# Kernel tuning notes

Measured on AMD Instinct MI355X. Metric: run time of the kernel, lower is better.

## Reference

```python
import jax, jax.numpy as jnp
import numpy as np

THRESH = 0.4


def setup_inputs() -> dict:
    key = jax.random.key(0)
    ks = jax.random.split(key, 8)
    B, N, C, H, O = 8, 16384, 640, 256, 128
    s = 0.02  # small init so sigmoid(logits) ~ 0.5 -> realistic mixed selection
    return {
        "point_features": jax.random.normal(ks[0], (B, N, C), jnp.float32),
        "point_coords": jax.random.normal(ks[1], (B, N, 3), jnp.float32) * 10.0,
        "w1": jax.random.normal(ks[2], (C, H), jnp.float32) * s,
        "b1": jnp.zeros((H,), jnp.float32),
        "w2": jax.random.normal(ks[3], (H, 1), jnp.float32) * s,
        "b2": jnp.zeros((1,), jnp.float32),
        "wo": jax.random.normal(ks[4], (C, O), jnp.float32) * s,
        "bo": jnp.zeros((O,), jnp.float32),
    }


def reference(point_features, point_coords, w1, b1, w2, b2, wo, bo):
    B, N, _ = point_features.shape
    # 2-layer MLP -> per-point logit -> sigmoid score
    h = jax.nn.relu(jnp.einsum('bnc,ch->bnh', point_features, w1) + b1)
    logits = jnp.einsum('bnh,ho->bno', h, w2) + b2          # [B, N, 1]
    scores = jax.nn.sigmoid(logits)                          # [B, N, 1]
    # score-scaled features through output projection
    feats = jnp.einsum('bnc,co->bno', point_features * scores, wo) + bo  # [B, N, O]
    # score-threshold selection + per-batch stream compaction into a
    # zero-padded tensor (padded to N, the jit-static worst case)
    sel = scores[..., 0] > THRESH                            # [B, N] bool
    pos = jnp.cumsum(sel.astype(jnp.int32), axis=1) - 1      # destination slot
    pos = jnp.where(sel, pos, N)                             # unselected -> OOB (dropped)
    bidx = jnp.arange(B)[:, None]
    selected_keypoints = jnp.zeros_like(feats).at[bidx, pos].set(feats, mode='drop')
    selected_coords = jnp.zeros_like(point_coords).at[bidx, pos].set(point_coords, mode='drop')
    # point_mask: True where the row is zero padding (matches (coords==0).sum(-1)!=0)
    point_mask = jnp.sum(selected_coords == 0, axis=-1) != 0
    return selected_keypoints, selected_coords, point_mask
```

## Files before the change

kernel.cpp:

```cpp
#include <hip/hip_runtime.h>
#include <hip/hip_bf16.h>


typedef __attribute__((ext_vector_type(8))) short short8v;
typedef __attribute__((ext_vector_type(4))) float f32x4;

#define M_TOTAL 131072
#define C_DIM 640
#define H_DIM 256
#define O_DIM 128
#define NCOMB 384
#define TM 64
#define KSTEPS 20
#define N_PTS 16384
#define TILES_PER_B 256
#define NTILES 2048
#define THRL -0.4054651081f
#define FIX_MARGIN 0.03f

#define OUT_COORD_OFF 16777216
#define OUT_MASK_OFF  17170432

#define WT_OFF     0u
#define TSTATE_OFF 491520u
#define TICKET_OFF 507904u
#define COUNTS_OFF 507908u

__device__ __forceinline__ int swzA(int u) {
  return u ^ (((u >> 3) & 1) | (((u >> 6) & 3) << 1));
}
__device__ __forceinline__ int swzB(int u) { return u ^ ((u >> 3) & 7); }

__device__ __forceinline__ void glds16(const void* g, void* l) {
  const __attribute__((address_space(1))) unsigned int* gp =
      reinterpret_cast<const __attribute__((address_space(1))) unsigned int*>(
          reinterpret_cast<uintptr_t>(g));
  __attribute__((address_space(3))) unsigned int* lp =
      reinterpret_cast<__attribute__((address_space(3))) unsigned int*>(
          reinterpret_cast<uintptr_t>(l));
  __builtin_amdgcn_global_load_lds(gp, lp, 16, 0, 0);
}

__device__ __forceinline__ unsigned int f2bf_bits(float f) {
  unsigned int u = __builtin_bit_cast(unsigned int, f);
  return (u + 0x7fffu + ((u >> 16) & 1u)) >> 16;
}
__device__ __forceinline__ unsigned int pack_bf2(float lo, float hi) {
  return f2bf_bits(lo) | (f2bf_bits(hi) << 16);
}

__global__ __launch_bounds__(256) void convert_w(const float* __restrict__ w1,
                                                 const float* __restrict__ wo,
                                                 unsigned short* __restrict__ Wt2,
                                                 unsigned long long* __restrict__ tstate,
                                                 int* __restrict__ ticket) {
  int o = blockIdx.x * 256 + threadIdx.x;
  if (o < NTILES) tstate[o] = 0ull;
  if (o == NTILES) *ticket = 0;
  if (o < NCOMB * C_DIM) {
    int e = o & 7;
    int chunk = o >> 3;
    int ks = chunk / 1536;
    int r = chunk - ks * 1536;
    int u = swzB(r);
    int n = u >> 2, kg = u & 3;
    int k = ks * 32 + kg * 8 + e;
    float v = (n < H_DIM) ? w1[k * H_DIM + n] : wo[k * O_DIM + (n - H_DIM)];
    Wt2[o] = (unsigned short)f2bf_bits(v);
  }
}

__global__ __launch_bounds__(512, 4) void gemm_fused(
    const float* __restrict__ pf, const unsigned short* __restrict__ Wt2,
    const float* __restrict__ w1, const float* __restrict__ b1,
    const float* __restrict__ w2, const float* __restrict__ b2,
    const float* __restrict__ pc, const float* __restrict__ bo,
    unsigned long long* __restrict__ tstate, int* __restrict__ ticket,
    int* __restrict__ counts, float* __restrict__ out) {
  __shared__ __align__(16) unsigned short As[2][256 * 8];
  __shared__ __align__(16) unsigned short Bs[2][1536 * 8];
  __shared__ float lpart[8][64];
  __shared__ float llog[64];
  __shared__ int dstrow[64];
  __shared__ float srow[64];
  __shared__ int s_tile;
  __shared__ unsigned long long s_fixmask;

  const int tid = threadIdx.x;
  const int lane = tid & 63;
  const int wv = tid >> 6;
  const int q = lane & 15;
  const int p = lane >> 4;

  if (tid == 0) s_tile = atomicAdd(ticket, 1);
  __syncthreads();
  const int tile = s_tile;
  const int m0 = tile * TM;

  f32x4 acc[3][4];
#pragma unroll
  for (int i = 0; i < 3; ++i)
#pragma unroll
    for (int rt = 0; rt < 4; ++rt) acc[i][rt] = (f32x4){0.f, 0.f, 0.f, 0.f};

  const int ar = tid >> 3;
  const int ah = tid & 7;
  const float* asrc = pf + (size_t)(m0 + ar) * C_DIM + ah * 4;
  const int awp = swzA(((ah >> 1) << 6) + ar) * 8 + (ah & 1) * 4;

  {
    float4 ra = *(const float4*)(asrc);
#pragma unroll
    for (int u = 0; u < 3; ++u)
      glds16(Wt2 + (size_t)(u * 512 + tid) * 8, &Bs[0][(u * 512 + tid) * 8]);
    *(uint2*)&As[0][awp] = make_uint2(pack_bf2(ra.x, ra.y), pack_bf2(ra.z, ra.w));
    __syncthreads();
  }

#pragma unroll 2
  for (int t = 0; t < KSTEPS; ++t) {
    const int cur = t & 1;
    float4 rn;
    if (t < KSTEPS - 1) {
      rn = *(const float4*)(asrc + (t + 1) * 32);
#pragma unroll
      for (int u = 0; u < 3; ++u)
        glds16(Wt2 + (size_t)((t + 1) * 1536 + u * 512 + tid) * 8,
               &Bs[cur ^ 1][(u * 512 + tid) * 8]);
    }
    short8v af[4];
#pragma unroll
    for (int rt = 0; rt < 4; ++rt)
      af[rt] = *(const short8v*)&As[cur][swzA((p << 6) + rt * 16 + q) * 8];
#pragma unroll
    for (int i = 0; i < 3; ++i) {
      const int ub = (((wv + 8 * i) * 16 + q) << 2) + p;
      short8v bfv = *(const short8v*)&Bs[cur][swzB(ub) * 8];
#pragma unroll
      for (int rt = 0; rt < 4; ++rt)
        acc[i][rt] = __builtin_amdgcn_mfma_f32_16x16x32_bf16(af[rt], bfv, acc[i][rt], 0, 0, 0);
    }
    if (t < KSTEPS - 1)
      *(uint2*)&As[cur ^ 1][awp] = make_uint2(pack_bf2(rn.x, rn.y), pack_bf2(rn.z, rn.w));
    __syncthreads();
  }

  float w2v[2], b1v[2];
#pragma unroll
  for (int i = 0; i < 2; ++i) {
    int col = (wv + 8 * i) * 16 + q;
    w2v[i] = w2[col];
    b1v[i] = b1[col];
  }
#pragma unroll
  for (int rt = 0; rt < 4; ++rt) {
    float pr[4] = {0.f, 0.f, 0.f, 0.f};
#pragma unroll
    for (int i = 0; i < 2; ++i)
#pragma unroll
      for (int r = 0; r < 4; ++r)
        pr[r] += fmaxf(acc[i][rt][r] + b1v[i], 0.f) * w2v[i];
#pragma unroll
    for (int mk = 1; mk < 16; mk <<= 1)
#pragma unroll
      for (int r = 0; r < 4; ++r) pr[r] += __shfl_xor(pr[r], mk);
    if (q == 0)
#pragma unroll
      for (int r = 0; r < 4; ++r) lpart[wv][rt * 16 + p * 4 + r] = pr[r];
  }
  __syncthreads();

  bool nf = false;
  if (wv == 0) {
    float lg = b2[0];
#pragma unroll
    for (int w = 0; w < 8; ++w) lg += lpart[w][tid];
    llog[tid] = lg;
    nf = fabsf(lg - THRL) < FIX_MARGIN;
  }
  unsigned long long fm = __ballot(nf);
  if (tid == 0) s_fixmask = fm;
  __syncthreads();

  unsigned long long fixmask = s_fixmask;
  while (fixmask) {
    int row = __ffsll(fixmask) - 1;
    fixmask &= fixmask - 1;
    if (tid < 256) {
      const float* prow = pf + (size_t)(m0 + row) * C_DIM;
      float a0 = 0.f, a1 = 0.f;
      for (int c = 0; c < C_DIM; c += 2) {
        a0 = fmaf(prow[c], w1[(size_t)c * H_DIM + tid], a0);
        a1 = fmaf(prow[c + 1], w1[(size_t)(c + 1) * H_DIM + tid], a1);
      }
      float v = fmaxf(a0 + a1 + b1[tid], 0.f) * w2[tid];
#pragma unroll
      for (int mk = 1; mk < 64; mk <<= 1) v += __shfl_xor(v, mk);
      if (lane == 0) lpart[0][wv] = v;
    }
    __syncthreads();
    if (tid == 0)
      llog[row] = lpart[0][0] + lpart[0][1] + lpart[0][2] + lpart[0][3] + b2[0];
    __syncthreads();
  }

  float flog = 0.f;
  bool sel = false;
  if (wv == 0) {
    flog = llog[tid];
    sel = flog > THRL;
  }
  unsigned long long selmask = __ballot(sel);
  if (wv == 0) {
    const int tb = tile & (TILES_PER_B - 1);
    const int cbase = tile - tb;
    int agg = __popcll(selmask);
    if (tid == 0) {
      unsigned long long fl = (tb == 0) ? 2ull : 1ull;
      __hip_atomic_store(&tstate[tile], (fl << 32) | (unsigned int)agg,
                         __ATOMIC_RELAXED, __HIP_MEMORY_SCOPE_AGENT);
    }
    int excl = 0;
    if (tb > 0) {
      int offset = tb - 1;
      while (true) {
        int idx = offset - tid;
        unsigned long long s = 0;
        if (idx >= 0) {
          do {
            s = __hip_atomic_load(&tstate[cbase + idx], __ATOMIC_RELAXED,
                                  __HIP_MEMORY_SCOPE_AGENT);
          } while (!(s >> 32));
        }
        unsigned flag = (unsigned)(s >> 32);
        unsigned long long pm = __ballot(flag == 2u);
        int val = (int)(s & 0xffffffffull);
        int contrib;
        if (pm) {
          int k = __ffsll(pm) - 1;
          contrib = (tid <= k) ? val : 0;
        } else {
          contrib = (idx >= 0) ? val : 0;
        }
#pragma unroll
        for (int mk = 1; mk < 64; mk <<= 1) contrib += __shfl_xor(contrib, mk);
        excl += contrib;
        if (pm) break;
        offset -= 64;
      }
      if (tid == 0)
        __hip_atomic_store(&tstate[tile], (2ull << 32) | (unsigned int)(excl + agg),
                           __ATOMIC_RELAXED, __HIP_MEMORY_SCOPE_AGENT);
    }
    int below = __popcll(selmask & ((1ull << tid) - 1ull));
    int bb = (tile >> 8) * N_PTS;
    dstrow[tid] = sel ? (bb + excl + below) : -1;
    srow[tid] = 1.f / (1.f + expf(-flog));
    if (tid == 0 && tb == TILES_PER_B - 1) counts[tile >> 8] = excl + agg;
  }
  __syncthreads();

  if (wv == 0 && dstrow[tid] >= 0) {
    int dst = dstrow[tid];
    int m = m0 + tid;
    float c0 = pc[m * 3], c1 = pc[m * 3 + 1], c2 = pc[m * 3 + 2];
    float* oc = out + OUT_COORD_OFF;
    oc[dst * 3] = c0; oc[dst * 3 + 1] = c1; oc[dst * 3 + 2] = c2;
    out[OUT_MASK_OFF + dst] = (c0 == 0.f || c1 == 0.f || c2 == 0.f) ? 1.f : 0.f;
  }

  {
    const int gcol = wv * 16 + q;
    const float bov = bo[gcol];
#pragma unroll
    for (int rt = 0; rt < 4; ++rt)
#pragma unroll
      for (int r = 0; r < 4; ++r) {
        int row = rt * 16 + p * 4 + r;
        int dst = dstrow[row];
        if (dst >= 0)
          out[(size_t)dst * O_DIM + gcol] = fmaf(acc[2][rt][r], srow[row], bov);
      }
  }
}

__global__ __launch_bounds__(256) void fill_tail(const int* __restrict__ counts,
                                                 float* __restrict__ out) {
  int m = blockIdx.x * 4 + (threadIdx.x >> 6);
  int lane = threadIdx.x & 63;
  int b = m >> 14, j = m & (N_PTS - 1);
  if (j < counts[b]) return;
  *(float2*)(out + (size_t)m * O_DIM + lane * 2) = make_float2(0.f, 0.f);
  if (lane == 0) {
    float* oc = out + OUT_COORD_OFF;
    oc[m * 3] = 0.f; oc[m * 3 + 1] = 0.f; oc[m * 3 + 2] = 0.f;
    out[OUT_MASK_OFF + m] = 1.f;
  }
}

extern "C" void kernel_launch(void* const* d_in, const int* in_sizes, int n_in,
                              void* d_out, int out_size, void* d_ws, size_t ws_size,
                              hipStream_t stream) {
  const float* pf = (const float*)d_in[0];
  const float* pc = (const float*)d_in[1];
  const float* w1 = (const float*)d_in[2];
  const float* b1 = (const float*)d_in[3];
  const float* w2 = (const float*)d_in[4];
  const float* b2 = (const float*)d_in[5];
  const float* wo = (const float*)d_in[6];
  const float* bo = (const float*)d_in[7];
  float* out = (float*)d_out;
  char* ws = (char*)d_ws;

  unsigned short* Wt2 = (unsigned short*)(ws + WT_OFF);
  unsigned long long* tstate = (unsigned long long*)(ws + TSTATE_OFF);
  int* ticket = (int*)(ws + TICKET_OFF);
  int* counts = (int*)(ws + COUNTS_OFF);

  convert_w<<<960, 256, 0, stream>>>(w1, wo, Wt2, tstate, ticket);
  gemm_fused<<<NTILES, 512, 0, stream>>>(pf, Wt2, w1, b1, w2, b2, pc, bo,
                                         tstate, ticket, counts, out);
  fill_tail<<<M_TOTAL / 4, 256, 0, stream>>>(counts, out);
}
```

Measured before the change: 219.4 us.

## Replace decoupled-lookback compaction with separate scan and scatter kernels

Result: faster. 200.4 us (-8.7%).

```diff
diff --git a/kernel.cpp b/kernel.cpp
--- a/kernel.cpp
+++ b/kernel.cpp
@@ -22,9 +22,11 @@
 #define OUT_MASK_OFF  17170432
 
 #define WT_OFF     0u
-#define TSTATE_OFF 491520u
-#define TICKET_OFF 507904u
-#define COUNTS_OFF 507908u
+#define TMASK_OFF  491520u
+#define TAGG_OFF   507904u
+#define TEXCL_OFF  516096u
+#define COUNTS_OFF 524288u
+#define G_OFF      1572864u
 
 __device__ __forceinline__ int swzA(int u) {
   return u ^ (((u >> 3) & 1) | (((u >> 6) & 3) << 1));
@@ -51,12 +53,8 @@
 
 __global__ __launch_bounds__(256) void convert_w(const float* __restrict__ w1,
                                                  const float* __restrict__ wo,
-                                                 unsigned short* __restrict__ Wt2,
-                                                 unsigned long long* __restrict__ tstate,
-                                                 int* __restrict__ ticket) {
+                                                 unsigned short* __restrict__ Wt2) {
   int o = blockIdx.x * 256 + threadIdx.x;
-  if (o < NTILES) tstate[o] = 0ull;
-  if (o == NTILES) *ticket = 0;
   if (o < NCOMB * C_DIM) {
     int e = o & 7;
     int chunk = o >> 3;
@@ -74,16 +72,13 @@
     const float* __restrict__ pf, const unsigned short* __restrict__ Wt2,
     const float* __restrict__ w1, const float* __restrict__ b1,
     const float* __restrict__ w2, const float* __restrict__ b2,
-    const float* __restrict__ pc, const float* __restrict__ bo,
-    unsigned long long* __restrict__ tstate, int* __restrict__ ticket,
-    int* __restrict__ counts, float* __restrict__ out) {
+    const float* __restrict__ bo, unsigned long long* __restrict__ tmask,
+    int* __restrict__ tagg, float* __restrict__ G) {
   __shared__ __align__(16) unsigned short As[2][256 * 8];
   __shared__ __align__(16) unsigned short Bs[2][1536 * 8];
   __shared__ float lpart[8][64];
   __shared__ float llog[64];
-  __shared__ int dstrow[64];
   __shared__ float srow[64];
-  __shared__ int s_tile;
   __shared__ unsigned long long s_fixmask;
 
   const int tid = threadIdx.x;
@@ -91,10 +86,7 @@
   const int wv = tid >> 6;
   const int q = lane & 15;
   const int p = lane >> 4;
-
-  if (tid == 0) s_tile = atomicAdd(ticket, 1);
-  __syncthreads();
-  const int tile = s_tile;
+  const int tile = blockIdx.x;
   const int m0 = tile * TM;
 
   f32x4 acc[3][4];
@@ -108,21 +100,23 @@
   const float* asrc = pf + (size_t)(m0 + ar) * C_DIM + ah * 4;
   const int awp = swzA(((ah >> 1) << 6) + ar) * 8 + (ah & 1) * 4;
 
+  float4 rB;
   {
-    float4 ra = *(const float4*)(asrc);
+    float4 rA = *(const float4*)(asrc);
+    rB = *(const float4*)(asrc + 32);
 #pragma unroll
     for (int u = 0; u < 3; ++u)
       glds16(Wt2 + (size_t)(u * 512 + tid) * 8, &Bs[0][(u * 512 + tid) * 8]);
-    *(uint2*)&As[0][awp] = make_uint2(pack_bf2(ra.x, ra.y), pack_bf2(ra.z, ra.w));
+    *(uint2*)&As[0][awp] = make_uint2(pack_bf2(rA.x, rA.y), pack_bf2(rA.z, rA.w));
     __syncthreads();
   }
 
 #pragma unroll 2
   for (int t = 0; t < KSTEPS; ++t) {
     const int cur = t & 1;
-    float4 rn;
-    if (t < KSTEPS - 1) {
-      rn = *(const float4*)(asrc + (t + 1) * 32);
+    float4 rC;
+    if (t + 2 < KSTEPS) rC = *(const float4*)(asrc + (t + 2) * 32);
+    if (t + 1 < KSTEPS) {
 #pragma unroll
       for (int u = 0; u < 3; ++u)
         glds16(Wt2 + (size_t)((t + 1) * 1536 + u * 512 + tid) * 8,
@@ -140,8 +134,9 @@
       for (int rt = 0; rt < 4; ++rt)
         acc[i][rt] = __builtin_amdgcn_mfma_f32_16x16x32_bf16(af[rt], bfv, acc[i][rt], 0, 0, 0);
     }
-    if (t < KSTEPS - 1)
-      *(uint2*)&As[cur ^ 1][awp] = make_uint2(pack_bf2(rn.x, rn.y), pack_bf2(rn.z, rn.w));
+    if (t + 1 < KSTEPS)
+      *(uint2*)&As[cur ^ 1][awp] = make_uint2(pack_bf2(rB.x, rB.y), pack_bf2(rB.z, rB.w));
+    rB = rC;
     __syncthreads();
   }
 
@@ -204,70 +199,21 @@
     __syncthreads();
   }
 
+  bool sel = false;
   float flog = 0.f;
-  bool sel = false;
   if (wv == 0) {
     flog = llog[tid];
     sel = flog > THRL;
   }
   unsigned long long selmask = __ballot(sel);
   if (wv == 0) {
-    const int tb = tile & (TILES_PER_B - 1);
-    const int cbase = tile - tb;
-    int agg = __popcll(selmask);
+    srow[tid] = 1.f / (1.f + expf(-flog));
     if (tid == 0) {
-      unsigned long long fl = (tb == 0) ? 2ull : 1ull;
-      __hip_atomic_store(&tstate[tile], (fl << 32) | (unsigned int)agg,
-                         __ATOMIC_RELAXED, __HIP_MEMORY_SCOPE_AGENT);
-    }
-    int excl = 0;
-    if (tb > 0) {
-      int offset = tb - 1;
-      while (true) {
-        int idx = offset - tid;
-        unsigned long long s = 0;
-        if (idx >= 0) {
-          do {
-            s = __hip_atomic_load(&tstate[cbase + idx], __ATOMIC_RELAXED,
-                                  __HIP_MEMORY_SCOPE_AGENT);
-          } while (!(s >> 32));
-        }
-        unsigned flag = (unsigned)(s >> 32);
-        unsigned long long pm = __ballot(flag == 2u);
-        int val = (int)(s & 0xffffffffull);
-        int contrib;
-        if (pm) {
-          int k = __ffsll(pm) - 1;
-          contrib = (tid <= k) ? val : 0;
-        } else {
-          contrib = (idx >= 0) ? val : 0;
-        }
-#pragma unroll
-        for (int mk = 1; mk < 64; mk <<= 1) contrib += __shfl_xor(contrib, mk);
-        excl += contrib;
-        if (pm) break;
-        offset -= 64;
-      }
-      if (tid == 0)
-        __hip_atomic_store(&tstate[tile], (2ull << 32) | (unsigned int)(excl + agg),
-                           __ATOMIC_RELAXED, __HIP_MEMORY_SCOPE_AGENT);
-    }
-    int below = __popcll(selmask & ((1ull << tid) - 1ull));
-    int bb = (tile >> 8) * N_PTS;
-    dstrow[tid] = sel ? (bb + excl + below) : -1;
-    srow[tid] = 1.f / (1.f + expf(-flog));
-    if (tid == 0 && tb == TILES_PER_B - 1) counts[tile >> 8] = excl + agg;
+      tmask[tile] = selmask;
+      tagg[tile] = __popcll(selmask);
+    }
   }
   __syncthreads();
-
-  if (wv == 0 && dstrow[tid] >= 0) {
-    int dst = dstrow[tid];
-    int m = m0 + tid;
-    float c0 = pc[m * 3], c1 = pc[m * 3 + 1], c2 = pc[m * 3 + 2];
-    float* oc = out + OUT_COORD_OFF;
-    oc[dst * 3] = c0; oc[dst * 3 + 1] = c1; oc[dst * 3 + 2] = c2;
-    out[OUT_MASK_OFF + dst] = (c0 == 0.f || c1 == 0.f || c2 == 0.f) ? 1.f : 0.f;
-  }
 
   {
     const int gcol = wv * 16 + q;
@@ -277,10 +223,59 @@
 #pragma unroll
       for (int r = 0; r < 4; ++r) {
         int row = rt * 16 + p * 4 + r;
-        int dst = dstrow[row];
-        if (dst >= 0)
-          out[(size_t)dst * O_DIM + gcol] = fmaf(acc[2][rt][r], srow[row], bov);
+        G[(size_t)(m0 + row) * O_DIM + gcol] = fmaf(acc[2][rt][r], srow[row], bov);
       }
+  }
+}
+
+__global__ __launch_bounds__(256) void scan_tiles(const int* __restrict__ tagg,
+                                                  int* __restrict__ texcl,
+                                                  int* __restrict__ counts) {
+  __shared__ int wsum[4];
+  const int c = blockIdx.x, t = threadIdx.x;
+  const int lane = t & 63, w = t >> 6;
+  int v = tagg[c * 256 + t];
+  int inc = v;
+#pragma unroll
+  for (int d = 1; d < 64; d <<= 1) {
+    int n = __shfl_up(inc, d);
+    if (lane >= d) inc += n;
+  }
+  if (lane == 63) wsum[w] = inc;
+  __syncthreads();
+  int base = 0;
+#pragma unroll
+  for (int ww = 0; ww < 4; ++ww)
+    if (ww < w) base += wsum[ww];
+  texcl[c * 256 + t] = base + inc - v;
+  if (t == 255) counts[c] = base + inc;
+}
+
+__global__ __launch_bounds__(512) void scatter(
+    const float* __restrict__ G, const unsigned long long* __restrict__ tmask,
+    const int* __restrict__ texcl, const float* __restrict__ pc,
+    float* __restrict__ out) {
+  const int tile = blockIdx.x;
+  const int tid = threadIdx.x;
+  const int lane = tid & 63;
+  const int wv = tid >> 6;
+  const unsigned long long mask = tmask[tile];
+  const int base = (tile >> 8) * N_PTS + texcl[tile];
+  const int m0 = tile * TM;
+#pragma unroll
+  for (int j = 0; j < 8; ++j) {
+    const int row = wv * 8 + j;
+    if (!((mask >> row) & 1ull)) continue;
+    const int dst = base + __popcll(mask & ((1ull << row) - 1ull));
+    const int m = m0 + row;
+    float2 g = *(const float2*)(G + (size_t)m * O_DIM + lane * 2);
+    *(float2*)(out + (size_t)dst * O_DIM + lane * 2) = g;
+    if (lane == 0) {
+      float c0 = pc[m * 3], c1 = pc[m * 3 + 1], c2 = pc[m * 3 + 2];
+      float* oc = out + OUT_COORD_OFF;
+      oc[dst * 3] = c0; oc[dst * 3 + 1] = c1; oc[dst * 3 + 2] = c2;
+      out[OUT_MASK_OFF + dst] = (c0 == 0.f || c1 == 0.f || c2 == 0.f) ? 1.f : 0.f;
+    }
   }
 }
 
@@ -313,12 +308,16 @@
   char* ws = (char*)d_ws;
 
   unsigned short* Wt2 = (unsigned short*)(ws + WT_OFF);
-  unsigned long long* tstate = (unsigned long long*)(ws + TSTATE_OFF);
-  int* ticket = (int*)(ws + TICKET_OFF);
+  unsigned long long* tmask = (unsigned long long*)(ws + TMASK_OFF);
+  int* tagg = (int*)(ws + TAGG_OFF);
+  int* texcl = (int*)(ws + TEXCL_OFF);
   int* counts = (int*)(ws + COUNTS_OFF);
-
-  convert_w<<<960, 256, 0, stream>>>(w1, wo, Wt2, tstate, ticket);
-  gemm_fused<<<NTILES, 512, 0, stream>>>(pf, Wt2, w1, b1, w2, b2, pc, bo,
-                                         tstate, ticket, counts, out);
+  float* G = (float*)(ws + G_OFF);
+
+  convert_w<<<960, 256, 0, stream>>>(w1, wo, Wt2);
+  gemm_fused<<<NTILES, 512, 0, stream>>>(pf, Wt2, w1, b1, w2, b2, bo,
+                                         tmask, tagg, G);
+  scan_tiles<<<8, 256, 0, stream>>>(tagg, texcl, counts);
+  scatter<<<NTILES, 512, 0, stream>>>(G, tmask, texcl, pc, out);
   fill_tail<<<M_TOTAL / 4, 256, 0, stream>>>(counts, out);
 }
```
